# Kernel tuning notes

Hardware: AMD Instinct MI355X
Metric: run time of the kernel (lower is better)

The kernel has to match this reference:

```python
import jax, jax.numpy as jnp
import numpy as np

EMB = 1024
HEADS = 16
HEAD_DIM = EMB // HEADS
D_FF = 4 * EMB
EPS = 1e-5


def setup_inputs() -> dict:
    key = jax.random.key(0)
    ks = jax.random.split(key, 12)
    b, t = 4, 2048
    sc = 0.02
    return {
        "x": jax.random.normal(ks[0], (b, t, EMB), dtype=jnp.float32),
        # weights stored [in, out] (transpose of torch Linear.weight)
        "w_attn": jax.random.normal(ks[1], (EMB, 3 * EMB), dtype=jnp.float32) * sc,
        "b_attn": jnp.zeros((3 * EMB,), dtype=jnp.float32),
        "w_proj": jax.random.normal(ks[2], (EMB, EMB), dtype=jnp.float32) * sc,
        "b_proj": jnp.zeros((EMB,), dtype=jnp.float32),
        "ln1_g": jnp.ones((EMB,), dtype=jnp.float32),
        "ln1_b": jnp.zeros((EMB,), dtype=jnp.float32),
        "w_ff1": jax.random.normal(ks[3], (EMB, D_FF), dtype=jnp.float32) * sc,
        "b_ff1": jnp.zeros((D_FF,), dtype=jnp.float32),
        "w_ff2": jax.random.normal(ks[4], (D_FF, EMB), dtype=jnp.float32) * sc,
        "b_ff2": jnp.zeros((EMB,), dtype=jnp.float32),
        "ln2_g": jnp.ones((EMB,), dtype=jnp.float32),
        "ln2_b": jnp.zeros((EMB,), dtype=jnp.float32),
    }


def _layernorm(x, g, b):
    mu = jnp.mean(x, axis=-1, keepdims=True)
    var = jnp.var(x, axis=-1, keepdims=True)
    return (x - mu) * jax.lax.rsqrt(var + EPS) * g + b


def reference(x, w_attn, b_attn, w_proj, b_proj, ln1_g, ln1_b,
              w_ff1, b_ff1, w_ff2, b_ff2, ln2_g, ln2_b):
    b, t, e = x.shape
    h, s = HEADS, HEAD_DIM
    # fused qkv projection (GPT2-style c_attn)
    qkv = x @ w_attn + b_attn                      # [b, t, 3e]
    q, k, v = jnp.split(qkv, 3, axis=-1)
    q = q.reshape(b, t, h, s).transpose(0, 2, 1, 3)  # [b, h, t, s]
    k = k.reshape(b, t, h, s).transpose(0, 2, 1, 3)
    v = v.reshape(b, t, h, s).transpose(0, 2, 1, 3)
    dot = jnp.einsum('bhqs,bhks->bhqk', q, k) / jnp.sqrt(jnp.float32(s))
    # causal mask: mask_(..., mask_diagonal=False) zeroes i < j (strict upper)
    causal = jnp.tril(jnp.ones((t, t), dtype=bool))
    dot = jnp.where(causal, dot, jnp.float32(-jnp.inf))
    att = jax.nn.softmax(dot, axis=-1)
    out = jnp.einsum('bhqk,bhks->bhqs', att, v)    # [b, h, t, s]
    out = out.transpose(0, 2, 1, 3).reshape(b, t, e)
    attended = out @ w_proj + b_proj
    # residual + LayerNorm (dropout is identity in eval mode)
    x1 = _layernorm(attended + x, ln1_g, ln1_b)
    ff = jax.nn.relu(x1 @ w_ff1 + b_ff1) @ w_ff2 + b_ff2
    return _layernorm(ff + x1, ln2_g, ln2_b)
```

## Files before the change

### kernel.cpp

```cpp
#include <hip/hip_runtime.h>
#include <hip/hip_bf16.h>


typedef __attribute__((ext_vector_type(8))) short bf16x8;
typedef __attribute__((ext_vector_type(4))) float f32x4;

__device__ __forceinline__ float b2f(unsigned short u) {
  return __uint_as_float(((unsigned int)u) << 16);
}
__device__ __forceinline__ unsigned short f2b(float f) {
  unsigned int u = __float_as_uint(f);
  u += 0x7fffu + ((u >> 16) & 1u);
  return (unsigned short)(u >> 16);
}
__device__ __forceinline__ void gload_lds16(const unsigned short* g, unsigned short* l) {
  __builtin_amdgcn_global_load_lds((const __attribute__((address_space(1))) void*)g,
                                   (__attribute__((address_space(3))) void*)l, 16, 0, 0);
}

__global__ __launch_bounds__(256) void cvt_bf16(const float* __restrict__ in,
                                                unsigned short* __restrict__ out, long n) {
  long i = ((long)blockIdx.x * 256 + threadIdx.x) * 4;
  if (i >= n) return;
  float4 v = *(const float4*)(in + i);
  *(ushort4*)(out + i) = make_ushort4(f2b(v.x), f2b(v.y), f2b(v.z), f2b(v.w));
}

__global__ __launch_bounds__(256) void transpose_bf16(const float* __restrict__ in,
                                                      unsigned short* __restrict__ out,
                                                      int R, int C) {
  __shared__ float tile[32][33];
  int c0 = blockIdx.x * 32, r0 = blockIdx.y * 32;
  for (int i = threadIdx.y; i < 32; i += 8)
    tile[i][threadIdx.x] = in[(long)(r0 + i) * C + c0 + threadIdx.x];
  __syncthreads();
  for (int i = threadIdx.y; i < 32; i += 8)
    out[(long)(c0 + i) * R + r0 + threadIdx.x] = f2b(tile[threadIdx.x][i]);
}

template <int EPI>
__global__ __launch_bounds__(256) void gemm_bf16(const unsigned short* __restrict__ A,
                                                 const unsigned short* __restrict__ Bt,
                                                 const float* __restrict__ bias,
                                                 void* __restrict__ Cout,
                                                 int M, int N, int K) {
  __shared__ unsigned short As[128 * 32];
  __shared__ unsigned short Bs[128 * 32];
  int t = threadIdx.x;
  int bm = blockIdx.x * 128, bn = blockIdx.y * 128;
  int w = t >> 6, lane = t & 63;
  int wr = w >> 1, wc = w & 1, quad = lane >> 4, l16 = lane & 15;
  int srow = t >> 2, scol = (t & 3) * 8;

  const unsigned short* Ap = A + (long)(bm + srow) * K + scol;
  const unsigned short* Bp = Bt + (long)(bn + srow) * K + scol;
  unsigned short* Asw = As + w * 512;
  unsigned short* Bsw = Bs + w * 512;

  f32x4 acc[4][4] = {};

  for (int k0 = 0; k0 < K; k0 += 32) {
    __syncthreads();
    gload_lds16(Ap + k0, Asw);
    gload_lds16(Ap + (long)64 * K + k0, Asw + 2048);
    gload_lds16(Bp + k0, Bsw);
    gload_lds16(Bp + (long)64 * K + k0, Bsw + 2048);
    __syncthreads();
    bf16x8 af[4], bfr[4];
#pragma unroll
    for (int i = 0; i < 4; ++i)
      af[i] = *(const bf16x8*)(As + (wr * 64 + i * 16 + l16) * 32 + quad * 8);
#pragma unroll
    for (int j = 0; j < 4; ++j)
      bfr[j] = *(const bf16x8*)(Bs + (wc * 64 + j * 16 + l16) * 32 + quad * 8);
#pragma unroll
    for (int i = 0; i < 4; ++i)
#pragma unroll
      for (int j = 0; j < 4; ++j)
        acc[i][j] = __builtin_amdgcn_mfma_f32_16x16x32_bf16(af[i], bfr[j], acc[i][j], 0, 0, 0);
  }

#pragma unroll
  for (int i = 0; i < 4; ++i) {
#pragma unroll
    for (int j = 0; j < 4; ++j) {
      int gn = bn + wc * 64 + j * 16 + l16;
      float bv = bias[gn];
      if (EPI == 3 && gn >= 2048) {
        int h = (gn >> 6) & 15, s = gn & 63;
        int gm0 = bm + wr * 64 + i * 16 + quad * 4;
        int b = gm0 >> 11, tt0 = gm0 & 2047;
        unsigned short* vt = (unsigned short*)Cout + 16777216L;
        ushort4 us;
        us.x = f2b(acc[i][j][0] + bv);
        us.y = f2b(acc[i][j][1] + bv);
        us.z = f2b(acc[i][j][2] + bv);
        us.w = f2b(acc[i][j][3] + bv);
        *(ushort4*)(vt + (((long)(b * 16 + h)) * 64 + s) * 2048 + tt0) = us;
      } else {
#pragma unroll
        for (int r = 0; r < 4; ++r) {
          int gm = bm + wr * 64 + i * 16 + quad * 4 + r;
          float v = acc[i][j][r] + bv;
          if (EPI == 2) v = fmaxf(v, 0.f);
          if (EPI == 0) {
            ((float*)Cout)[(long)gm * N + gn] = v;
          } else if (EPI == 1 || EPI == 2) {
            ((unsigned short*)Cout)[(long)gm * N + gn] = f2b(v);
          } else {
            float sc = (gn < 1024) ? 0.18033688011112042f : 1.0f;
            ((unsigned short*)Cout)[(long)gm * 2048 + gn] = f2b(v * sc);
          }
        }
      }
    }
  }
}

__global__ __launch_bounds__(256) void attn_mfma(const unsigned short* __restrict__ qkv,
                                                 unsigned short* __restrict__ outp) {
  const int LD = 72;
  __shared__ unsigned short Qs[64 * LD];
  __shared__ unsigned short Ks[64 * LD];
  __shared__ unsigned short Vts[64 * LD];
  __shared__ unsigned short Ps[64 * LD];
  int qi = blockIdx.x, h = blockIdx.y, b = blockIdx.z;
  int t = threadIdx.x;
  int w = t >> 6, lane = t & 63, quad = lane >> 4, l16 = lane & 15;
  int q0 = qi * 64;
  const unsigned short* qg = qkv + (long)(b * 2048) * 2048 + h * 64;
  const unsigned short* kg = qg + 1024;
  const unsigned short* vg = qkv + 16777216L + (((long)(b * 16 + h)) * 64) * 2048;

  int sr = t >> 2, sc = (t & 3) * 16;
  {
    const unsigned short* qp = qg + (long)(q0 + sr) * 2048 + sc;
    *(int4*)(Qs + sr * LD + sc) = *(const int4*)qp;
    *(int4*)(Qs + sr * LD + sc + 8) = *(const int4*)(qp + 8);
  }

  f32x4 oacc[4] = {};
  f32x4 lacc = {};
  const short ONE = 0x3F80;
  bf16x8 ones = {ONE, ONE, ONE, ONE, ONE, ONE, ONE, ONE};

  int4 kv0, kv1, vv0, vv1;
  {
    const unsigned short* kp = kg + (long)sr * 2048 + sc;
    const unsigned short* vp = vg + (long)sr * 2048 + sc;
    kv0 = *(const int4*)kp; kv1 = *(const int4*)(kp + 8);
    vv0 = *(const int4*)vp; vv1 = *(const int4*)(vp + 8);
  }

  for (int kt = 0; kt <= qi; ++kt) {
    __syncthreads();
    *(int4*)(Ks + sr * LD + sc) = kv0;
    *(int4*)(Ks + sr * LD + sc + 8) = kv1;
    *(int4*)(Vts + sr * LD + sc) = vv0;
    *(int4*)(Vts + sr * LD + sc + 8) = vv1;
    __syncthreads();
    if (kt < qi) {
      const unsigned short* kp = kg + (long)((kt + 1) * 64 + sr) * 2048 + sc;
      const unsigned short* vp = vg + (long)sr * 2048 + (kt + 1) * 64 + sc;
      kv0 = *(const int4*)kp; kv1 = *(const int4*)(kp + 8);
      vv0 = *(const int4*)vp; vv1 = *(const int4*)(vp + 8);
    }

    f32x4 sacc[4] = {};
#pragma unroll
    for (int ks = 0; ks < 2; ++ks) {
      bf16x8 aq = *(const bf16x8*)(Qs + (w * 16 + l16) * LD + ks * 32 + quad * 8);
#pragma unroll
      for (int j = 0; j < 4; ++j) {
        bf16x8 bk = *(const bf16x8*)(Ks + (j * 16 + l16) * LD + ks * 32 + quad * 8);
        sacc[j] = __builtin_amdgcn_mfma_f32_16x16x32_bf16(aq, bk, sacc[j], 0, 0, 0);
      }
    }
    if (kt == qi) {
#pragma unroll
      for (int j = 0; j < 4; ++j)
#pragma unroll
        for (int r = 0; r < 4; ++r)
          if (j * 16 + l16 > w * 16 + quad * 4 + r) sacc[j][r] = -1e30f;
    }
#pragma unroll
    for (int j = 0; j < 4; ++j)
#pragma unroll
      for (int r = 0; r < 4; ++r)
        Ps[(w * 16 + quad * 4 + r) * LD + j * 16 + l16] = f2b(exp2f(sacc[j][r]));

#pragma unroll
    for (int ks = 0; ks < 2; ++ks) {
      bf16x8 ap = *(const bf16x8*)(Ps + (w * 16 + l16) * LD + ks * 32 + quad * 8);
      lacc = __builtin_amdgcn_mfma_f32_16x16x32_bf16(ap, ones, lacc, 0, 0, 0);
#pragma unroll
      for (int j2 = 0; j2 < 4; ++j2) {
        bf16x8 bv = *(const bf16x8*)(Vts + (j2 * 16 + l16) * LD + ks * 32 + quad * 8);
        oacc[j2] = __builtin_amdgcn_mfma_f32_16x16x32_bf16(ap, bv, oacc[j2], 0, 0, 0);
      }
    }
  }

#pragma unroll
  for (int r = 0; r < 4; ++r) {
    float invl = 1.f / lacc[r];
    int row = q0 + w * 16 + quad * 4 + r;
    unsigned short* op = outp + ((long)(b * 2048 + row)) * 1024 + h * 64;
#pragma unroll
    for (int j2 = 0; j2 < 4; ++j2) op[j2 * 16 + l16] = f2b(oacc[j2][r] * invl);
  }
}

__global__ __launch_bounds__(256) void ln_kernel(const float* __restrict__ a,
                                                 const float* __restrict__ res,
                                                 const float* __restrict__ gam,
                                                 const float* __restrict__ bet,
                                                 float* __restrict__ outf,
                                                 unsigned short* __restrict__ outb) {
  int row = blockIdx.x, t = threadIdx.x;
  float4 av = *(const float4*)(a + (long)row * 1024 + t * 4);
  float4 rv = *(const float4*)(res + (long)row * 1024 + t * 4);
  float v0 = av.x + rv.x, v1 = av.y + rv.y, v2 = av.z + rv.z, v3 = av.w + rv.w;
  float s = v0 + v1 + v2 + v3;
  float ss = v0 * v0 + v1 * v1 + v2 * v2 + v3 * v3;
#pragma unroll
  for (int off = 32; off >= 1; off >>= 1) {
    s += __shfl_down(s, off);
    ss += __shfl_down(ss, off);
  }
  __shared__ float sb[4], ssb[4];
  __shared__ float mean_s, inv_s;
  int w = t >> 6, lane = t & 63;
  if (lane == 0) { sb[w] = s; ssb[w] = ss; }
  __syncthreads();
  if (t == 0) {
    float S = sb[0] + sb[1] + sb[2] + sb[3];
    float SS = ssb[0] + ssb[1] + ssb[2] + ssb[3];
    float mean = S * (1.f / 1024.f);
    float var = SS * (1.f / 1024.f) - mean * mean;
    mean_s = mean;
    inv_s = rsqrtf(var + 1e-5f);
  }
  __syncthreads();
  float mean = mean_s, inv = inv_s;
  int c = t * 4;
  float4 gv = *(const float4*)(gam + c);
  float4 bv = *(const float4*)(bet + c);
  float y0 = (v0 - mean) * inv * gv.x + bv.x;
  float y1 = (v1 - mean) * inv * gv.y + bv.y;
  float y2 = (v2 - mean) * inv * gv.z + bv.z;
  float y3 = (v3 - mean) * inv * gv.w + bv.w;
  *(float4*)(outf + (long)row * 1024 + c) = make_float4(y0, y1, y2, y3);
  if (outb) {
    *(ushort4*)(outb + (long)row * 1024 + c) = make_ushort4(f2b(y0), f2b(y1), f2b(y2), f2b(y3));
  }
}

extern "C" void kernel_launch(void* const* d_in, const int* in_sizes, int n_in,
                              void* d_out, int out_size, void* d_ws, size_t ws_size,
                              hipStream_t stream) {
  const float* x      = (const float*)d_in[0];
  const float* w_attn = (const float*)d_in[1];
  const float* b_attn = (const float*)d_in[2];
  const float* w_proj = (const float*)d_in[3];
  const float* b_proj = (const float*)d_in[4];
  const float* ln1_g  = (const float*)d_in[5];
  const float* ln1_b  = (const float*)d_in[6];
  const float* w_ff1  = (const float*)d_in[7];
  const float* b_ff1  = (const float*)d_in[8];
  const float* w_ff2  = (const float*)d_in[9];
  const float* b_ff2  = (const float*)d_in[10];
  const float* ln2_g  = (const float*)d_in[11];
  const float* ln2_b  = (const float*)d_in[12];

  const long M = 8192, E = 1024;
  char* ws = (char*)d_ws;
  unsigned short* xb   = (unsigned short*)ws; ws += M * E * 2;
  unsigned short* wTa  = (unsigned short*)ws; ws += 3072L * 1024 * 2;
  unsigned short* wTp  = (unsigned short*)ws; ws += 1024L * 1024 * 2;
  unsigned short* wTf1 = (unsigned short*)ws; ws += 4096L * 1024 * 2;
  unsigned short* wTf2 = (unsigned short*)ws; ws += 4096L * 1024 * 2;
  unsigned short* qkvb = (unsigned short*)ws; ws += M * 3072 * 2;
  unsigned short* attb = (unsigned short*)ws; ws += M * E * 2;
  float* a1f = (float*)ws; ws += M * E * 4;
  float* x1f = (float*)ws; ws += M * E * 4;
  unsigned short* x1b = (unsigned short*)ws; ws += M * E * 2;
  unsigned short* hb = qkvb;
  float* f2 = a1f;

  cvt_bf16<<<dim3((M * E) / 4 / 256), dim3(256), 0, stream>>>(x, xb, M * E);
  transpose_bf16<<<dim3(3072 / 32, 1024 / 32), dim3(32, 8), 0, stream>>>(w_attn, wTa, 1024, 3072);
  transpose_bf16<<<dim3(1024 / 32, 1024 / 32), dim3(32, 8), 0, stream>>>(w_proj, wTp, 1024, 1024);
  transpose_bf16<<<dim3(4096 / 32, 1024 / 32), dim3(32, 8), 0, stream>>>(w_ff1, wTf1, 1024, 4096);
  transpose_bf16<<<dim3(1024 / 32, 4096 / 32), dim3(32, 8), 0, stream>>>(w_ff2, wTf2, 4096, 1024);
  gemm_bf16<3><<<dim3(64, 24), dim3(256), 0, stream>>>(xb, wTa, b_attn, qkvb, 8192, 3072, 1024);
  attn_mfma<<<dim3(32, 16, 4), dim3(256), 0, stream>>>(qkvb, attb);
  gemm_bf16<0><<<dim3(64, 8), dim3(256), 0, stream>>>(attb, wTp, b_proj, a1f, 8192, 1024, 1024);
  ln_kernel<<<dim3(8192), dim3(256), 0, stream>>>(a1f, x, ln1_g, ln1_b, x1f, x1b);
  gemm_bf16<2><<<dim3(64, 32), dim3(256), 0, stream>>>(x1b, wTf1, b_ff1, hb, 8192, 4096, 1024);
  gemm_bf16<0><<<dim3(64, 8), dim3(256), 0, stream>>>(hb, wTf2, b_ff2, f2, 8192, 1024, 4096);
  ln_kernel<<<dim3(8192), dim3(256), 0, stream>>>(f2, x1f, ln2_g, ln2_b, (float*)d_out, nullptr);
}
```

Before: 610.4 us.

## Restructure attention so each wave owns 32 query rows and loads K/V directly

The attention kernel now gives each wave its own 32 query rows (128 rows per block), keeps Q fragments in registers, and loads K and V fragments straight from global memory into registers instead of staging them through shared LDS tiles with block-wide barriers. S is computed transposed (K as the A operand), so the exp'd probabilities go into a per-wave P buffer with packed 8-byte writes. Diagonal tiles skip the fully masked half of the work. This removes __syncthreads and LDS round-trips and reduces redundant causal work. In exchange, waves in a block no longer share K/V loads, which raises global/L2 traffic, and there is no explicit prefetch of the next tile.

```diff
diff --git a/kernel.cpp b/kernel.cpp
--- a/kernel.cpp
+++ b/kernel.cpp
@@ -120,95 +120,96 @@
 __global__ __launch_bounds__(256) void attn_mfma(const unsigned short* __restrict__ qkv,
                                                  unsigned short* __restrict__ outp) {
   const int LD = 72;
-  __shared__ unsigned short Qs[64 * LD];
-  __shared__ unsigned short Ks[64 * LD];
-  __shared__ unsigned short Vts[64 * LD];
-  __shared__ unsigned short Ps[64 * LD];
-  int qi = blockIdx.x, h = blockIdx.y, b = blockIdx.z;
+  __shared__ __align__(16) unsigned short Ps[4][32 * LD];
+  int h = blockIdx.y, b = blockIdx.z;
   int t = threadIdx.x;
   int w = t >> 6, lane = t & 63, quad = lane >> 4, l16 = lane & 15;
-  int q0 = qi * 64;
+  int q0 = blockIdx.x * 128 + w * 32;
   const unsigned short* qg = qkv + (long)(b * 2048) * 2048 + h * 64;
   const unsigned short* kg = qg + 1024;
   const unsigned short* vg = qkv + 16777216L + (((long)(b * 16 + h)) * 64) * 2048;
-
-  int sr = t >> 2, sc = (t & 3) * 16;
-  {
-    const unsigned short* qp = qg + (long)(q0 + sr) * 2048 + sc;
-    *(int4*)(Qs + sr * LD + sc) = *(const int4*)qp;
-    *(int4*)(Qs + sr * LD + sc + 8) = *(const int4*)(qp + 8);
-  }
-
-  f32x4 oacc[4] = {};
-  f32x4 lacc = {};
+  unsigned short* Pw = &Ps[w][0];
+
+  bf16x8 qf[2][2];
+#pragma unroll
+  for (int g = 0; g < 2; ++g)
+#pragma unroll
+    for (int ks = 0; ks < 2; ++ks)
+      qf[g][ks] = *(const bf16x8*)(qg + (long)(q0 + g * 16 + l16) * 2048 + ks * 32 + quad * 8);
+
+  f32x4 oacc[2][4] = {};
+  f32x4 lacc[2] = {};
   const short ONE = 0x3F80;
   bf16x8 ones = {ONE, ONE, ONE, ONE, ONE, ONE, ONE, ONE};
 
-  int4 kv0, kv1, vv0, vv1;
-  {
-    const unsigned short* kp = kg + (long)sr * 2048 + sc;
-    const unsigned short* vp = vg + (long)sr * 2048 + sc;
-    kv0 = *(const int4*)kp; kv1 = *(const int4*)(kp + 8);
-    vv0 = *(const int4*)vp; vv1 = *(const int4*)(vp + 8);
-  }
-
-  for (int kt = 0; kt <= qi; ++kt) {
-    __syncthreads();
-    *(int4*)(Ks + sr * LD + sc) = kv0;
-    *(int4*)(Ks + sr * LD + sc + 8) = kv1;
-    *(int4*)(Vts + sr * LD + sc) = vv0;
-    *(int4*)(Vts + sr * LD + sc + 8) = vv1;
-    __syncthreads();
-    if (kt < qi) {
-      const unsigned short* kp = kg + (long)((kt + 1) * 64 + sr) * 2048 + sc;
-      const unsigned short* vp = vg + (long)sr * 2048 + (kt + 1) * 64 + sc;
-      kv0 = *(const int4*)kp; kv1 = *(const int4*)(kp + 8);
-      vv0 = *(const int4*)vp; vv1 = *(const int4*)(vp + 8);
+  int lastkt = (q0 + 31) >> 6;
+  for (int kt = 0; kt <= lastkt; ++kt) {
+    bool diag = (kt == lastkt);
+    int rgmax = (diag && ((q0 & 63) == 0)) ? 2 : 4;
+    int kcmax = rgmax >> 1;
+
+    bf16x8 kf[4][2];
+#pragma unroll
+    for (int rg = 0; rg < 4; ++rg) {
+      if (rg >= rgmax) break;
+#pragma unroll
+      for (int ks = 0; ks < 2; ++ks)
+        kf[rg][ks] = *(const bf16x8*)(kg + (long)(kt * 64 + rg * 16 + l16) * 2048 + ks * 32 + quad * 8);
     }
-
-    f32x4 sacc[4] = {};
-#pragma unroll
-    for (int ks = 0; ks < 2; ++ks) {
-      bf16x8 aq = *(const bf16x8*)(Qs + (w * 16 + l16) * LD + ks * 32 + quad * 8);
-#pragma unroll
-      for (int j = 0; j < 4; ++j) {
-        bf16x8 bk = *(const bf16x8*)(Ks + (j * 16 + l16) * LD + ks * 32 + quad * 8);
-        sacc[j] = __builtin_amdgcn_mfma_f32_16x16x32_bf16(aq, bk, sacc[j], 0, 0, 0);
+    bf16x8 vf[4][2];
+#pragma unroll
+    for (int sg = 0; sg < 4; ++sg)
+#pragma unroll
+      for (int kc = 0; kc < 2; ++kc) {
+        if (kc >= kcmax) break;
+        vf[sg][kc] = *(const bf16x8*)(vg + (long)(sg * 16 + l16) * 2048 + kt * 64 + kc * 32 + quad * 8);
+      }
+
+#pragma unroll
+    for (int rg = 0; rg < 4; ++rg) {
+      if (rg >= rgmax) break;
+#pragma unroll
+      for (int cg = 0; cg < 2; ++cg) {
+        f32x4 st = {};
+#pragma unroll
+        for (int ks = 0; ks < 2; ++ks)
+          st = __builtin_amdgcn_mfma_f32_16x16x32_bf16(kf[rg][ks], qf[cg][ks], st, 0, 0, 0);
+        if (diag) {
+          int qg_ = q0 + cg * 16 + l16;
+          int kb = kt * 64 + rg * 16 + quad * 4;
+#pragma unroll
+          for (int r = 0; r < 4; ++r)
+            if (kb + r > qg_) st[r] = -1e30f;
+        }
+        unsigned int lo = ((unsigned int)f2b(exp2f(st[1])) << 16) | f2b(exp2f(st[0]));
+        unsigned int hi = ((unsigned int)f2b(exp2f(st[3])) << 16) | f2b(exp2f(st[2]));
+        *(uint2*)(Pw + (cg * 16 + l16) * LD + rg * 16 + quad * 4) = make_uint2(lo, hi);
       }
     }
-    if (kt == qi) {
-#pragma unroll
-      for (int j = 0; j < 4; ++j)
-#pragma unroll
-        for (int r = 0; r < 4; ++r)
-          if (j * 16 + l16 > w * 16 + quad * 4 + r) sacc[j][r] = -1e30f;
+
+#pragma unroll
+    for (int g = 0; g < 2; ++g)
+#pragma unroll
+      for (int kc = 0; kc < 2; ++kc) {
+        if (kc >= kcmax) break;
+        bf16x8 ap = *(const bf16x8*)(Pw + (g * 16 + l16) * LD + kc * 32 + quad * 8);
+        lacc[g] = __builtin_amdgcn_mfma_f32_16x16x32_bf16(ap, ones, lacc[g], 0, 0, 0);
+#pragma unroll
+        for (int sg = 0; sg < 4; ++sg)
+          oacc[g][sg] = __builtin_amdgcn_mfma_f32_16x16x32_bf16(ap, vf[sg][kc], oacc[g][sg], 0, 0, 0);
+      }
+  }
+
+#pragma unroll
+  for (int g = 0; g < 2; ++g)
+#pragma unroll
+    for (int r = 0; r < 4; ++r) {
+      float invl = 1.f / lacc[g][r];
+      int row = q0 + g * 16 + quad * 4 + r;
+      unsigned short* op = outp + ((long)(b * 2048 + row)) * 1024 + h * 64;
+#pragma unroll
+      for (int sg = 0; sg < 4; ++sg) op[sg * 16 + l16] = f2b(oacc[g][sg][r] * invl);
     }
-#pragma unroll
-    for (int j = 0; j < 4; ++j)
-#pragma unroll
-      for (int r = 0; r < 4; ++r)
-        Ps[(w * 16 + quad * 4 + r) * LD + j * 16 + l16] = f2b(exp2f(sacc[j][r]));
-
-#pragma unroll
-    for (int ks = 0; ks < 2; ++ks) {
-      bf16x8 ap = *(const bf16x8*)(Ps + (w * 16 + l16) * LD + ks * 32 + quad * 8);
-      lacc = __builtin_amdgcn_mfma_f32_16x16x32_bf16(ap, ones, lacc, 0, 0, 0);
-#pragma unroll
-      for (int j2 = 0; j2 < 4; ++j2) {
-        bf16x8 bv = *(const bf16x8*)(Vts + (j2 * 16 + l16) * LD + ks * 32 + quad * 8);
-        oacc[j2] = __builtin_amdgcn_mfma_f32_16x16x32_bf16(ap, bv, oacc[j2], 0, 0, 0);
-      }
-    }
-  }
-
-#pragma unroll
-  for (int r = 0; r < 4; ++r) {
-    float invl = 1.f / lacc[r];
-    int row = q0 + w * 16 + quad * 4 + r;
-    unsigned short* op = outp + ((long)(b * 2048 + row)) * 1024 + h * 64;
-#pragma unroll
-    for (int j2 = 0; j2 < 4; ++j2) op[j2 * 16 + l16] = f2b(oacc[j2][r] * invl);
-  }
 }
 
 __global__ __launch_bounds__(256) void ln_kernel(const float* __restrict__ a,
@@ -294,7 +295,7 @@
   transpose_bf16<<<dim3(4096 / 32, 1024 / 32), dim3(32, 8), 0, stream>>>(w_ff1, wTf1, 1024, 4096);
   transpose_bf16<<<dim3(1024 / 32, 4096 / 32), dim3(32, 8), 0, stream>>>(w_ff2, wTf2, 4096, 1024);
   gemm_bf16<3><<<dim3(64, 24), dim3(256), 0, stream>>>(xb, wTa, b_attn, qkvb, 8192, 3072, 1024);
-  attn_mfma<<<dim3(32, 16, 4), dim3(256), 0, stream>>>(qkvb, attb);
+  attn_mfma<<<dim3(16, 16, 4), dim3(256), 0, stream>>>(qkvb, attb);
   gemm_bf16<0><<<dim3(64, 8), dim3(256), 0, stream>>>(attb, wTp, b_proj, a1f, 8192, 1024, 1024);
   ln_kernel<<<dim3(8192), dim3(256), 0, stream>>>(a1f, x, ln1_g, ln1_b, x1f, x1b);
   gemm_bf16<2><<<dim3(64, 32), dim3(256), 0, stream>>>(x1b, wTf1, b_ff1, hb, 8192, 4096, 1024);
```

After: 727.7 us. 19.2% more time.

## Restructure attention tile: transposed S, per-wave P buffer, skip masked diagonal work

Applied to the files above, without the earlier changes.

The attention kernel now computes S transposed (K as the A operand, Q as B), so each lane writes a packed 4-element row segment of P into a private per-wave LDS buffer instead of scattered scalar stores. On the diagonal tile, each wave skips the fully masked 16-column groups and 32-wide PV chunks, zero-filling the padding it still reads. Q fragments are hoisted into registers before the loop, and blocks are launched in reverse order so the longest causal rows start first. This cuts LDS store traffic and masked-out MFMA work, in exchange for more complex diagonal-tile control flow.

```diff
diff --git a/kernel.cpp b/kernel.cpp
--- a/kernel.cpp
+++ b/kernel.cpp
@@ -120,17 +120,19 @@
 __global__ __launch_bounds__(256) void attn_mfma(const unsigned short* __restrict__ qkv,
                                                  unsigned short* __restrict__ outp) {
   const int LD = 72;
-  __shared__ unsigned short Qs[64 * LD];
-  __shared__ unsigned short Ks[64 * LD];
-  __shared__ unsigned short Vts[64 * LD];
-  __shared__ unsigned short Ps[64 * LD];
-  int qi = blockIdx.x, h = blockIdx.y, b = blockIdx.z;
+  __shared__ __align__(16) unsigned short Qs[64 * LD];
+  __shared__ __align__(16) unsigned short Ks[64 * LD];
+  __shared__ __align__(16) unsigned short Vts[64 * LD];
+  __shared__ __align__(16) unsigned short Ps[4][16 * LD];
+  int qi = 31 - blockIdx.x;
+  int h = blockIdx.y, b = blockIdx.z;
   int t = threadIdx.x;
   int w = t >> 6, lane = t & 63, quad = lane >> 4, l16 = lane & 15;
   int q0 = qi * 64;
   const unsigned short* qg = qkv + (long)(b * 2048) * 2048 + h * 64;
   const unsigned short* kg = qg + 1024;
   const unsigned short* vg = qkv + 16777216L + (((long)(b * 16 + h)) * 64) * 2048;
+  unsigned short* Pw = &Ps[w][0];
 
   int sr = t >> 2, sc = (t & 3) * 16;
   {
@@ -138,12 +140,6 @@
     *(int4*)(Qs + sr * LD + sc) = *(const int4*)qp;
     *(int4*)(Qs + sr * LD + sc + 8) = *(const int4*)(qp + 8);
   }
-
-  f32x4 oacc[4] = {};
-  f32x4 lacc = {};
-  const short ONE = 0x3F80;
-  bf16x8 ones = {ONE, ONE, ONE, ONE, ONE, ONE, ONE, ONE};
-
   int4 kv0, kv1, vv0, vv1;
   {
     const unsigned short* kp = kg + (long)sr * 2048 + sc;
@@ -151,6 +147,15 @@
     kv0 = *(const int4*)kp; kv1 = *(const int4*)(kp + 8);
     vv0 = *(const int4*)vp; vv1 = *(const int4*)(vp + 8);
   }
+  bf16x8 qf[2];
+#pragma unroll
+  for (int ks = 0; ks < 2; ++ks)
+    qf[ks] = *(const bf16x8*)(Qs + (w * 16 + l16) * LD + ks * 32 + quad * 8);
+
+  f32x4 oacc[4] = {};
+  f32x4 lacc = {};
+  const short ONE = 0x3F80;
+  bf16x8 ones = {ONE, ONE, ONE, ONE, ONE, ONE, ONE, ONE};
 
   for (int kt = 0; kt <= qi; ++kt) {
     __syncthreads();
@@ -166,37 +171,40 @@
       vv0 = *(const int4*)vp; vv1 = *(const int4*)(vp + 8);
     }
 
-    f32x4 sacc[4] = {};
-#pragma unroll
-    for (int ks = 0; ks < 2; ++ks) {
-      bf16x8 aq = *(const bf16x8*)(Qs + (w * 16 + l16) * LD + ks * 32 + quad * 8);
-#pragma unroll
-      for (int j = 0; j < 4; ++j) {
-        bf16x8 bk = *(const bf16x8*)(Ks + (j * 16 + l16) * LD + ks * 32 + quad * 8);
-        sacc[j] = __builtin_amdgcn_mfma_f32_16x16x32_bf16(aq, bk, sacc[j], 0, 0, 0);
+    bool diag = (kt == qi);
+    int rgmax = diag ? (w + 1) : 4;
+    int kcmax = diag ? ((w >> 1) + 1) : 2;
+    if (diag && !(w & 1))
+      *(uint2*)(Pw + l16 * LD + rgmax * 16 + quad * 4) = make_uint2(0u, 0u);
+
+#pragma unroll
+    for (int rg = 0; rg < 4; ++rg) {
+      if (rg >= rgmax) break;
+      f32x4 st = {};
+#pragma unroll
+      for (int ks = 0; ks < 2; ++ks) {
+        bf16x8 kf = *(const bf16x8*)(Ks + (rg * 16 + l16) * LD + ks * 32 + quad * 8);
+        st = __builtin_amdgcn_mfma_f32_16x16x32_bf16(kf, qf[ks], st, 0, 0, 0);
       }
+      if (diag && rg + 1 == rgmax) {
+#pragma unroll
+        for (int r = 0; r < 4; ++r)
+          if (quad * 4 + r > l16) st[r] = -1e30f;
+      }
+      unsigned int lo = ((unsigned int)f2b(exp2f(st[1])) << 16) | f2b(exp2f(st[0]));
+      unsigned int hi = ((unsigned int)f2b(exp2f(st[3])) << 16) | f2b(exp2f(st[2]));
+      *(uint2*)(Pw + l16 * LD + rg * 16 + quad * 4) = make_uint2(lo, hi);
     }
-    if (kt == qi) {
-#pragma unroll
-      for (int j = 0; j < 4; ++j)
-#pragma unroll
-        for (int r = 0; r < 4; ++r)
-          if (j * 16 + l16 > w * 16 + quad * 4 + r) sacc[j][r] = -1e30f;
-    }
-#pragma unroll
-    for (int j = 0; j < 4; ++j)
-#pragma unroll
-      for (int r = 0; r < 4; ++r)
-        Ps[(w * 16 + quad * 4 + r) * LD + j * 16 + l16] = f2b(exp2f(sacc[j][r]));
-
-#pragma unroll
-    for (int ks = 0; ks < 2; ++ks) {
-      bf16x8 ap = *(const bf16x8*)(Ps + (w * 16 + l16) * LD + ks * 32 + quad * 8);
+
+#pragma unroll
+    for (int kc = 0; kc < 2; ++kc) {
+      if (kc >= kcmax) break;
+      bf16x8 ap = *(const bf16x8*)(Pw + l16 * LD + kc * 32 + quad * 8);
       lacc = __builtin_amdgcn_mfma_f32_16x16x32_bf16(ap, ones, lacc, 0, 0, 0);
 #pragma unroll
-      for (int j2 = 0; j2 < 4; ++j2) {
-        bf16x8 bv = *(const bf16x8*)(Vts + (j2 * 16 + l16) * LD + ks * 32 + quad * 8);
-        oacc[j2] = __builtin_amdgcn_mfma_f32_16x16x32_bf16(ap, bv, oacc[j2], 0, 0, 0);
+      for (int sg = 0; sg < 4; ++sg) {
+        bf16x8 vf = *(const bf16x8*)(Vts + (sg * 16 + l16) * LD + kc * 32 + quad * 8);
+        oacc[sg] = __builtin_amdgcn_mfma_f32_16x16x32_bf16(ap, vf, oacc[sg], 0, 0, 0);
       }
     }
   }
@@ -207,7 +215,7 @@
     int row = q0 + w * 16 + quad * 4 + r;
     unsigned short* op = outp + ((long)(b * 2048 + row)) * 1024 + h * 64;
 #pragma unroll
-    for (int j2 = 0; j2 < 4; ++j2) op[j2 * 16 + l16] = f2b(oacc[j2][r] * invl);
+    for (int sg = 0; sg < 4; ++sg) op[sg * 16 + l16] = f2b(oacc[sg][r] * invl);
   }
 }
 
```

After: 632.9 us. 3.7% more time.
